# Kernel optimization log

Hardware: AMD Instinct MI355X
Metric: run time of the kernel (lower is better)

The kernel has to match this reference:

```python
import jax, jax.numpy as jnp
import numpy as np

B, SQ, SKV = 4, 4096, 1024
QDIM, CDIM = 1024, 768
HEADS, DHEAD = 16, 64
INNER = HEADS * DHEAD


def setup_inputs() -> dict:
    key = jax.random.key(0)
    ks = jax.random.split(key, 7)
    s = 0.02
    return {
        "x": jax.random.normal(ks[0], (B, SQ, QDIM), dtype=jnp.float32),
        "context": jax.random.normal(ks[1], (B, SKV, CDIM), dtype=jnp.float32),
        "Wq": jax.random.normal(ks[2], (QDIM, INNER), dtype=jnp.float32) * s,
        "Wk": jax.random.normal(ks[3], (CDIM, INNER), dtype=jnp.float32) * s,
        "Wv": jax.random.normal(ks[4], (CDIM, INNER), dtype=jnp.float32) * s,
        "Wo": jax.random.normal(ks[5], (INNER, QDIM), dtype=jnp.float32) * s,
        "bo": jnp.zeros((QDIM,), dtype=jnp.float32),
    }


def reference(x, context, Wq, Wk, Wv, Wo, bo):
    # QKV projections (no bias, matching bias=False Linear layers)
    q = x @ Wq          # [B, SQ, INNER]
    k = context @ Wk    # [B, SKV, INNER]
    v = context @ Wv    # [B, SKV, INNER]

    # split heads: b s (h d) -> b h s d
    def split_heads(t, s):
        return t.reshape(B, s, HEADS, DHEAD).transpose(0, 2, 1, 3)

    qh = split_heads(q, SQ)
    kh = split_heads(k, SKV)
    vh = split_heads(v, SKV)

    scale = DHEAD ** -0.5  # attention_basic default scale
    sim = jnp.einsum('bhqd,bhkd->bhqk', qh, kh) * scale  # [B,H,SQ,SKV]
    attn = jax.nn.softmax(sim, axis=-1)
    out = jnp.einsum('bhqk,bhkd->bhqd', attn, vh)        # [B,H,SQ,DHEAD]
    out = out.transpose(0, 2, 1, 3).reshape(B, SQ, INNER)

    # output projection (Linear with bias); dropout p=0 -> identity
    return out @ Wo + bo
```

## Files before the change

### kernel.cpp

```cpp
#include <hip/hip_runtime.h>


typedef unsigned short u16;
typedef __bf16 bf16x8 __attribute__((ext_vector_type(8)));
typedef float float4v __attribute__((ext_vector_type(4)));
typedef _Float16 half4 __attribute__((ext_vector_type(4)));
typedef _Float16 half2v __attribute__((ext_vector_type(2)));
typedef __attribute__((address_space(1))) void as1_void;
typedef __attribute__((address_space(3))) void as3_void;

__device__ __forceinline__ u16 f2bf(float f) {
  unsigned u = __float_as_uint(f);
  u += 0x7FFF + ((u >> 16) & 1);
  return (u16)(u >> 16);
}

__device__ __forceinline__ void async16(const u16* g, u16* l) {
  __builtin_amdgcn_global_load_lds((as1_void*)(void*)g, (as3_void*)l, 16, 0, 0);
}

#define WAITCNT_VM8 0xF78
#define WAITCNT_VM4 0xF74
#define WAITCNT_VM0 0xF70

__global__ void cvt_kernel(const float* __restrict__ x, u16* __restrict__ xbf,
                           const float* __restrict__ ctx, u16* __restrict__ ctxbf) {
  int i = blockIdx.x * 256 + threadIdx.x;
  const float* in; u16* out; int j;
  if (i < 4194304) { in = x; out = xbf; j = i; }
  else if (i < 4980736) { in = ctx; out = ctxbf; j = i - 4194304; }
  else return;
  float4 v = ((const float4*)in)[j];
  ushort4 o;
  o.x = f2bf(v.x); o.y = f2bf(v.y); o.z = f2bf(v.z); o.w = f2bf(v.w);
  ((ushort4*)out)[j] = o;
}

__global__ void twt_kernel(const float* __restrict__ Wq, const float* __restrict__ Wk,
                           const float* __restrict__ Wv, const float* __restrict__ Wo,
                           u16* __restrict__ WqT, u16* __restrict__ WkT,
                           u16* __restrict__ WvT, u16* __restrict__ WoT) {
  __shared__ u16 t[32][33];
  int z = blockIdx.z;
  const float* W = z == 0 ? Wq : z == 1 ? Wk : z == 2 ? Wv : Wo;
  u16* Wt = z == 0 ? WqT : z == 1 ? WkT : z == 2 ? WvT : WoT;
  int Kd = (z == 1 || z == 2) ? 768 : 1024;
  int k0 = blockIdx.y * 32;
  if (k0 >= Kd) return;
  int tx = threadIdx.x, ty = threadIdx.y;
  int n0 = blockIdx.x * 32;
#pragma unroll
  for (int i = 0; i < 4; i++)
    t[ty + i * 8][tx] = f2bf(W[(size_t)(k0 + ty + i * 8) * 1024 + n0 + tx]);
  __syncthreads();
#pragma unroll
  for (int i = 0; i < 4; i++)
    Wt[(size_t)(n0 + ty + i * 8) * Kd + k0 + tx] = t[tx][ty + i * 8];
}


__device__ __forceinline__ void ld_a4(const u16 (*Lp)[256][8], int rbase, int quad,
                                      int l15, bf16x8 a[4][2]) {
#pragma unroll
  for (int mi = 0; mi < 4; mi++)
#pragma unroll
    for (int ks = 0; ks < 2; ks++)
      a[mi][ks] = *(const bf16x8*)&Lp[ks * 4 + quad][rbase + mi * 16 + l15][0];
}

__device__ __forceinline__ void ld_b2(const u16 (*Lp)[256][8], int rbase, int quad,
                                      int l15, bf16x8 b[2][2]) {
#pragma unroll
  for (int ni = 0; ni < 2; ni++)
#pragma unroll
    for (int ks = 0; ks < 2; ks++)
      b[ni][ks] = *(const bf16x8*)&Lp[ks * 4 + quad][rbase + ni * 16 + l15][0];
}

__device__ __forceinline__ void mm16(bf16x8 a[4][2], bf16x8 b[2][2],
                                     float4v acc[8][4], int mh, int nh) {
  __builtin_amdgcn_s_setprio(1);
#pragma unroll
  for (int mi = 0; mi < 4; mi++)
#pragma unroll
    for (int ni = 0; ni < 2; ni++)
#pragma unroll
      for (int ks = 0; ks < 2; ks++)
        acc[mh * 4 + mi][nh * 2 + ni] = __builtin_amdgcn_mfma_f32_16x16x32_bf16(
            a[mi][ks], b[ni][ks], acc[mh * 4 + mi][nh * 2 + ni], 0, 0, 0);
  __builtin_amdgcn_s_setprio(0);
}

__device__ __forceinline__ void gemm256_core(const u16* __restrict__ A,
                                             const u16* __restrict__ Bt, int K,
                                             int m0, int n0, float4v acc[8][4]) {
  __shared__ __align__(16) u16 L[2][2][8][256][8];
  int tid = threadIdx.x;
  int w = tid >> 6, lane = tid & 63;
  int l15 = lane & 15, quad = lane >> 4;
  int wm = (w >> 2) * 128, wn = (w & 3) * 64;

  int c0 = 2 * w, c1 = 2 * w + 1;
  int kc0 = c0 & 7, mb0 = (c0 >> 3) * 64;
  int kc1 = c1 & 7, mb1 = (c1 >> 3) * 64;
  const u16* pA0 = A + (size_t)(m0 + mb0 + lane) * K + kc0 * 8;
  const u16* pA1 = A + (size_t)(m0 + mb1 + lane) * K + kc1 * 8;
  const u16* pB0 = Bt + (size_t)(n0 + mb0 + lane) * K + kc0 * 8;
  const u16* pB1 = Bt + (size_t)(n0 + mb1 + lane) * K + kc1 * 8;
  size_t hs = (size_t)128 * K;

#define STG_A(buf, t)                                                          \
  do {                                                                         \
    const u16* s0 = pA0 + (size_t)(t) * 64;                                    \
    const u16* s1 = pA1 + (size_t)(t) * 64;                                    \
    async16(s0, &L[buf][0][kc0][mb0][0]);                                      \
    async16(s1, &L[buf][0][kc1][mb1][0]);                                      \
    async16(s0 + hs, &L[buf][0][kc0][128 + mb0][0]);                           \
    async16(s1 + hs, &L[buf][0][kc1][128 + mb1][0]);                           \
  } while (0)
#define STG_B(buf, t)                                                          \
  do {                                                                         \
    const u16* s0 = pB0 + (size_t)(t) * 64;                                    \
    const u16* s1 = pB1 + (size_t)(t) * 64;                                    \
    async16(s0, &L[buf][1][kc0][mb0][0]);                                      \
    async16(s1, &L[buf][1][kc1][mb1][0]);                                      \
    async16(s0 + hs, &L[buf][1][kc0][128 + mb0][0]);                           \
    async16(s1 + hs, &L[buf][1][kc1][128 + mb1][0]);                           \
  } while (0)

  STG_A(0, 0); STG_B(0, 0);
  STG_A(1, 1); STG_B(1, 1);
  __builtin_amdgcn_s_waitcnt(WAITCNT_VM8);
  __builtin_amdgcn_s_barrier();

  bf16x8 a[4][2], b0[2][2], b1[2][2];
  int I = K >> 7;
  for (int i = 0; i < I; ++i) {
    int st = (i + 1 < I);
    ld_a4(L[0][0], wm, quad, l15, a);
    ld_b2(L[0][1], wn, quad, l15, b0);
    if (i > 0) STG_B(1, 2 * i + 1);
    __builtin_amdgcn_s_barrier();
    mm16(a, b0, acc, 0, 0);
    __builtin_amdgcn_s_barrier();
    ld_b2(L[0][1], wn + 32, quad, l15, b1);
    __builtin_amdgcn_s_barrier();
    mm16(a, b1, acc, 0, 1);
    __builtin_amdgcn_s_barrier();
    ld_a4(L[0][0], wm + 64, quad, l15, a);
    __builtin_amdgcn_s_barrier();
    mm16(a, b1, acc, 1, 1);
    __builtin_amdgcn_s_barrier();
    if (st) STG_A(0, 2 * i + 2);
    __builtin_amdgcn_s_barrier();
    mm16(a, b0, acc, 1, 0);
    if (st) __builtin_amdgcn_s_waitcnt(WAITCNT_VM4);
    else    __builtin_amdgcn_s_waitcnt(WAITCNT_VM0);
    __builtin_amdgcn_s_barrier();
    ld_a4(L[1][0], wm, quad, l15, a);
    ld_b2(L[1][1], wn, quad, l15, b0);
    if (st) STG_B(0, 2 * i + 2);
    __builtin_amdgcn_s_barrier();
    mm16(a, b0, acc, 0, 0);
    __builtin_amdgcn_s_barrier();
    ld_b2(L[1][1], wn + 32, quad, l15, b1);
    __builtin_amdgcn_s_barrier();
    mm16(a, b1, acc, 0, 1);
    __builtin_amdgcn_s_barrier();
    ld_a4(L[1][0], wm + 64, quad, l15, a);
    __builtin_amdgcn_s_barrier();
    mm16(a, b1, acc, 1, 1);
    __builtin_amdgcn_s_barrier();
    if (st) STG_A(1, 2 * i + 3);
    __builtin_amdgcn_s_barrier();
    mm16(a, b0, acc, 1, 0);
    if (st) __builtin_amdgcn_s_waitcnt(WAITCNT_VM4);
    __builtin_amdgcn_s_barrier();
  }
#undef STG_A
#undef STG_B
}

__global__ __launch_bounds__(512, 2) void qkv_gemm8(
    const u16* __restrict__ xbf, const u16* __restrict__ ctxbf,
    const u16* __restrict__ WqT, const u16* __restrict__ WkT, const u16* __restrict__ WvT,
    u16* __restrict__ Qb, u16* __restrict__ Kbuf, u16* __restrict__ Vtb, float qscale) {
  int bx = blockIdx.x;
  const u16* A; const u16* Bt; u16* C; int K, mode, m0, n0; float scale;
  if (bx < 256)      { int t = bx;       A = xbf;   Bt = WqT; C = Qb;   K = 1024; mode = 0; scale = qscale; m0 = (t >> 2) * 256; n0 = (t & 3) * 256; }
  else if (bx < 320) { int t = bx - 256; A = ctxbf; Bt = WkT; C = Kbuf; K = 768;  mode = 0; scale = 1.0f;   m0 = (t >> 2) * 256; n0 = (t & 3) * 256; }
  else               { int t = bx - 320; A = ctxbf; Bt = WvT; C = Vtb;  K = 768;  mode = 2; scale = 1.0f;   m0 = (t >> 2) * 256; n0 = (t & 3) * 256; }

  float4v acc[8][4] = {};
  gemm256_core(A, Bt, K, m0, n0, acc);

  int tid = threadIdx.x;
  int w = tid >> 6, lane = tid & 63;
  int l15 = lane & 15, quad = lane >> 4;
  int wm = (w >> 2) * 128, wn = (w & 3) * 64;

  if (mode == 0) {
#pragma unroll
    for (int mi = 0; mi < 8; mi++) {
      int rowb = m0 + wm + mi * 16 + quad * 4;
#pragma unroll
      for (int ni = 0; ni < 4; ni++) {
        int col = n0 + wn + ni * 16 + l15;
#pragma unroll
        for (int r = 0; r < 4; r++)
          C[(size_t)(rowb + r) * 1024 + col] = f2bf(acc[mi][ni][r] * scale);
      }
    }
  } else {
#pragma unroll
    for (int mi = 0; mi < 8; mi++) {
      int rowb = m0 + wm + mi * 16 + quad * 4;
#pragma unroll
      for (int ni = 0; ni < 4; ni++) {
        int col = n0 + wn + ni * 16 + l15;
        int hh = col >> 6, dd = col & 63;
#pragma unroll
        for (int r = 0; r < 4; r++) {
          int rr = rowb + r;
          int b = rr >> 10, skv = rr & 1023;
          _Float16 hv = (_Float16)acc[mi][ni][r];
          C[((((size_t)b * 16 + hh) * 64 + dd) << 10) + skv] = __builtin_bit_cast(u16, hv);
        }
      }
    }
  }
}

__global__ __launch_bounds__(512, 2) void gemm_bt8(
    const u16* __restrict__ A, const u16* __restrict__ Bt,
    float* __restrict__ C, const float* __restrict__ bias) {
  int bx = blockIdx.x;
  int m0 = (bx >> 2) * 256, n0 = (bx & 3) * 256;

  float4v acc[8][4] = {};
  gemm256_core(A, Bt, 1024, m0, n0, acc);

  int tid = threadIdx.x;
  int w = tid >> 6, lane = tid & 63;
  int l15 = lane & 15, quad = lane >> 4;
  int wm = (w >> 2) * 128, wn = (w & 3) * 64;

#pragma unroll
  for (int mi = 0; mi < 8; mi++) {
    int rowb = m0 + wm + mi * 16 + quad * 4;
#pragma unroll
    for (int ni = 0; ni < 4; ni++) {
      int col = n0 + wn + ni * 16 + l15;
      float bv = bias[col];
#pragma unroll
      for (int r = 0; r < 4; r++)
        C[(size_t)(rowb + r) * 1024 + col] = acc[mi][ni][r] + bv;
    }
  }
}

__global__ __launch_bounds__(512, 4) void attn_kernel(
    const u16* __restrict__ Q, const u16* __restrict__ Kb,
    const u16* __restrict__ Vt, u16* __restrict__ Oout) {
  __shared__ __align__(16) u16 lK[2][4096];
  __shared__ __align__(16) u16 lV[2][4096];
  int tid = threadIdx.x, w = tid >> 6, lane = tid & 63;
  int l15 = lane & 15, quad = lane >> 4;
  int bh = blockIdx.y, b = bh >> 4, h = bh & 15;
  int q0 = blockIdx.x * 256 + w * 32;

  const u16* Qbase = Q + ((size_t)(b * 4096 + q0)) * 1024 + h * 64;
  const u16* Kbase = Kb + ((size_t)b << 20) + h * 64;
  const u16* Vbase = Vt + ((size_t)bh << 16);

  bf16x8 qf[2][2];
#pragma unroll
  for (int qt = 0; qt < 2; qt++)
#pragma unroll
    for (int c = 0; c < 2; c++)
      qf[qt][c] = *(const bf16x8*)(Qbase + (size_t)(qt * 16 + l15) * 1024 + c * 32 + quad * 8);

  int x0 = ((tid & 7) ^ ((tid >> 3) & 7)) * 8, r0 = (tid >> 3) * 1024;
  const u16* ks0 = Kbase + r0 + x0;
  const u16* vs0 = Vbase + r0 + x0;
  int kdo0 = w * 512;

  async16(ks0, &lK[0][kdo0]);
  async16(vs0, &lV[0][kdo0]);
  ks0 += 65536;
  vs0 += 64;

  float4v o[2][4] = {};
  float4v osum[2] = {};
  const half4 ones = {(_Float16)1.0f, (_Float16)1.0f, (_Float16)1.0f, (_Float16)1.0f};

  int lb = l15 & 7;
  int xk0 = ((0 + quad) ^ lb) * 16 + l15 * 128;
  int xk1 = ((4 + quad) ^ lb) * 16 + l15 * 128;
  int qh = quad >> 1, qo = (quad & 1) * 8;
  int vrow = l15 * 128 + qo;

  for (int it = 0; it < 16; ++it) {
    const char* bK = (const char*)lK + (it & 1) * 8192;
    const char* bV = (const char*)lV + (it & 1) * 8192;
    __syncthreads();
    if (it < 15) {
      int nb = (it + 1) & 1;
      async16(ks0, &lK[nb][kdo0]);
      async16(vs0, &lV[nb][kdo0]);
      ks0 += 65536;
      vs0 += 64;
    }
#pragma unroll
    for (int ss = 0; ss < 4; ss++) {
      int sub = (ss + w) & 3;
      int sb = sub * 2048;
      float4v sv[2] = {{0.f, 0.f, 0.f, 0.f}, {0.f, 0.f, 0.f, 0.f}};
      __builtin_amdgcn_s_setprio(1);
#pragma unroll
      for (int c = 0; c < 2; c++) {
        bf16x8 kf = *(const bf16x8*)(bK + sb + (c ? xk1 : xk0));
#pragma unroll
        for (int qt = 0; qt < 2; qt++)
          sv[qt] = __builtin_amdgcn_mfma_f32_16x16x32_bf16(kf, qf[qt][c], sv[qt], 0, 0, 0);
      }
      __builtin_amdgcn_s_setprio(0);
      half4 pf[2];
#pragma unroll
      for (int qt = 0; qt < 2; qt++) {
        float e0 = exp2f(sv[qt][0]), e1 = exp2f(sv[qt][1]);
        float e2 = exp2f(sv[qt][2]), e3 = exp2f(sv[qt][3]);
        half2v p01 = __builtin_bit_cast(half2v, __builtin_amdgcn_cvt_pkrtz(e0, e1));
        half2v p23 = __builtin_bit_cast(half2v, __builtin_amdgcn_cvt_pkrtz(e2, e3));
        pf[qt] = __builtin_shufflevector(p01, p23, 0, 1, 2, 3);
        osum[qt] = __builtin_amdgcn_mfma_f32_16x16x16f16(ones, pf[qt], osum[qt], 0, 0, 0);
      }
      int vbs = vrow + (((sub * 2 + qh) ^ lb) * 16);
      __builtin_amdgcn_s_setprio(1);
#pragma unroll
      for (int dt = 0; dt < 4; dt++) {
        half4 vf = *(const half4*)(bV + dt * 2048 + vbs);
#pragma unroll
        for (int qt = 0; qt < 2; qt++)
          o[qt][dt] = __builtin_amdgcn_mfma_f32_16x16x16f16(vf, pf[qt], o[qt][dt], 0, 0, 0);
      }
      __builtin_amdgcn_s_setprio(0);
    }
  }

#pragma unroll
  for (int qt = 0; qt < 2; qt++) {
    float inv = 1.0f / osum[qt][0];
    u16* Ob = Oout + ((size_t)(b * 4096 + q0 + qt * 16 + l15)) * 1024 + h * 64 + quad * 4;
#pragma unroll
    for (int dt = 0; dt < 4; dt++) {
      ushort4 pk;
      pk.x = f2bf(o[qt][dt][0] * inv);
      pk.y = f2bf(o[qt][dt][1] * inv);
      pk.z = f2bf(o[qt][dt][2] * inv);
      pk.w = f2bf(o[qt][dt][3] * inv);
      *(ushort4*)(Ob + dt * 16) = pk;
    }
  }
}

extern "C" void kernel_launch(void* const* d_in, const int* in_sizes, int n_in,
                              void* d_out, int out_size, void* d_ws, size_t ws_size,
                              hipStream_t stream) {
  const float* x   = (const float*)d_in[0];
  const float* ctx = (const float*)d_in[1];
  const float* Wq  = (const float*)d_in[2];
  const float* Wk  = (const float*)d_in[3];
  const float* Wv  = (const float*)d_in[4];
  const float* Wo  = (const float*)d_in[5];
  const float* bo  = (const float*)d_in[6];
  float* out = (float*)d_out;

  u16* ws    = (u16*)d_ws;
  u16* xbf   = ws;
  u16* ctxbf = xbf + 16777216;
  u16* WqT   = ctxbf + 3145728;
  u16* WkT   = WqT + 1048576;
  u16* WvT   = WkT + 786432;
  u16* WoT   = WvT + 786432;
  u16* Qb    = WoT + 1048576;
  u16* Kbuf  = Qb + 16777216;
  u16* Vtb   = Kbuf + 4194304;
  if (ws_size < (size_t)48758784 * 2) return;

  cvt_kernel<<<19456, 256, 0, stream>>>(x, xbf, ctx, ctxbf);
  twt_kernel<<<dim3(32, 32, 4), dim3(32, 8), 0, stream>>>(Wq, Wk, Wv, Wo, WqT, WkT, WvT, WoT);
  qkv_gemm8<<<dim3(384), dim3(512), 0, stream>>>(xbf, ctxbf, WqT, WkT, WvT,
                                                 Qb, Kbuf, Vtb, 0.18033688011112042f);
  attn_kernel<<<dim3(16, 64), dim3(512), 0, stream>>>(Qb, Kbuf, Vtb, xbf);
  gemm_bt8<<<dim3(256), dim3(512), 0, stream>>>(xbf, WoT, out, bo);
}
```

Baseline: 395.2 us.

## Use 16x16x32 f16 MFMA for PV by permuting P fragments across lanes

Pairs of 16-key subtiles are merged so the P@V and row-sum products use the K=32 f16 MFMA instead of two K=16 MFMAs. Since the QK output layout does not match the K=32 operand layout, P values are rearranged across lanes with ds_bpermute and a per-lane select, and V is loaded as 8-wide fragments. This halves the number of PV MFMA issues but adds 16 bpermutes per step. It also drops the per-wave staggered subtile order.

```diff
diff --git a/kernel.cpp b/kernel.cpp
--- a/kernel.cpp
+++ b/kernel.cpp
@@ -2,10 +2,14 @@
 
 
 typedef unsigned short u16;
+typedef unsigned int u32;
 typedef __bf16 bf16x8 __attribute__((ext_vector_type(8)));
 typedef float float4v __attribute__((ext_vector_type(4)));
 typedef _Float16 half4 __attribute__((ext_vector_type(4)));
+typedef _Float16 half8 __attribute__((ext_vector_type(8)));
 typedef _Float16 half2v __attribute__((ext_vector_type(2)));
+typedef u32 u32x2 __attribute__((ext_vector_type(2)));
+typedef u32 u32x4 __attribute__((ext_vector_type(4)));
 typedef __attribute__((address_space(1))) void as1_void;
 typedef __attribute__((address_space(3))) void as3_void;
 
@@ -292,13 +296,16 @@
 
   float4v o[2][4] = {};
   float4v osum[2] = {};
-  const half4 ones = {(_Float16)1.0f, (_Float16)1.0f, (_Float16)1.0f, (_Float16)1.0f};
+  const half8 ones8 = {(_Float16)1.0f, (_Float16)1.0f, (_Float16)1.0f, (_Float16)1.0f,
+                       (_Float16)1.0f, (_Float16)1.0f, (_Float16)1.0f, (_Float16)1.0f};
 
   int lb = l15 & 7;
   int xk0 = ((0 + quad) ^ lb) * 16 + l15 * 128;
   int xk1 = ((4 + quad) ^ lb) * 16 + l15 * 128;
-  int qh = quad >> 1, qo = (quad & 1) * 8;
-  int vrow = l15 * 128 + qo;
+  int vrow = l15 * 128;
+  int idx_lo = (((quad & 1) << 5) + l15) << 2;
+  int idx_hi = idx_lo + 64;
+  bool useb = (quad & 2) != 0;
 
   for (int it = 0; it < 16; ++it) {
     const char* bK = (const char*)lK + (it & 1) * 8192;
@@ -312,37 +319,60 @@
       vs0 += 64;
     }
 #pragma unroll
-    for (int ss = 0; ss < 4; ss++) {
-      int sub = (ss + w) & 3;
-      int sb = sub * 2048;
-      float4v sv[2] = {{0.f, 0.f, 0.f, 0.f}, {0.f, 0.f, 0.f, 0.f}};
+    for (int s = 0; s < 2; ++s) {
+      half4 pp[2][2];
+#pragma unroll
+      for (int hp = 0; hp < 2; ++hp) {
+        int sub = s * 2 + hp;
+        const char* kb = bK + sub * 2048;
+        float4v sv[2] = {{0.f, 0.f, 0.f, 0.f}, {0.f, 0.f, 0.f, 0.f}};
+        __builtin_amdgcn_s_setprio(1);
+#pragma unroll
+        for (int c = 0; c < 2; c++) {
+          bf16x8 kf = *(const bf16x8*)(kb + (c ? xk1 : xk0));
+#pragma unroll
+          for (int qt = 0; qt < 2; qt++)
+            sv[qt] = __builtin_amdgcn_mfma_f32_16x16x32_bf16(kf, qf[qt][c], sv[qt], 0, 0, 0);
+        }
+        __builtin_amdgcn_s_setprio(0);
+#pragma unroll
+        for (int qt = 0; qt < 2; qt++) {
+          float e0 = exp2f(sv[qt][0]), e1 = exp2f(sv[qt][1]);
+          float e2 = exp2f(sv[qt][2]), e3 = exp2f(sv[qt][3]);
+          half2v p01 = __builtin_bit_cast(half2v, __builtin_amdgcn_cvt_pkrtz(e0, e1));
+          half2v p23 = __builtin_bit_cast(half2v, __builtin_amdgcn_cvt_pkrtz(e2, e3));
+          pp[hp][qt] = __builtin_shufflevector(p01, p23, 0, 1, 2, 3);
+        }
+      }
+      half8 p8s[2];
+#pragma unroll
+      for (int qt = 0; qt < 2; qt++) {
+        u32x2 a2 = __builtin_bit_cast(u32x2, pp[0][qt]);
+        u32x2 b2 = __builtin_bit_cast(u32x2, pp[1][qt]);
+        int al0 = __builtin_amdgcn_ds_bpermute(idx_lo, (int)a2[0]);
+        int ah0 = __builtin_amdgcn_ds_bpermute(idx_lo, (int)a2[1]);
+        int al1 = __builtin_amdgcn_ds_bpermute(idx_hi, (int)a2[0]);
+        int ah1 = __builtin_amdgcn_ds_bpermute(idx_hi, (int)a2[1]);
+        int bl0 = __builtin_amdgcn_ds_bpermute(idx_lo, (int)b2[0]);
+        int bh0 = __builtin_amdgcn_ds_bpermute(idx_lo, (int)b2[1]);
+        int bl1 = __builtin_amdgcn_ds_bpermute(idx_hi, (int)b2[0]);
+        int bh1 = __builtin_amdgcn_ds_bpermute(idx_hi, (int)b2[1]);
+        u32x4 od;
+        od[0] = (u32)(useb ? bl0 : al0);
+        od[1] = (u32)(useb ? bh0 : ah0);
+        od[2] = (u32)(useb ? bl1 : al1);
+        od[3] = (u32)(useb ? bh1 : ah1);
+        half8 p8 = __builtin_bit_cast(half8, od);
+        p8s[qt] = p8;
+        osum[qt] = __builtin_amdgcn_mfma_f32_16x16x32_f16(ones8, p8, osum[qt], 0, 0, 0);
+      }
       __builtin_amdgcn_s_setprio(1);
 #pragma unroll
-      for (int c = 0; c < 2; c++) {
-        bf16x8 kf = *(const bf16x8*)(bK + sb + (c ? xk1 : xk0));
+      for (int dt = 0; dt < 4; dt++) {
+        half8 vf = *(const half8*)(bV + dt * 2048 + vrow + (((s * 4 + quad) ^ lb) * 16));
 #pragma unroll
         for (int qt = 0; qt < 2; qt++)
-          sv[qt] = __builtin_amdgcn_mfma_f32_16x16x32_bf16(kf, qf[qt][c], sv[qt], 0, 0, 0);
-      }
-      __builtin_amdgcn_s_setprio(0);
-      half4 pf[2];
-#pragma unroll
-      for (int qt = 0; qt < 2; qt++) {
-        float e0 = exp2f(sv[qt][0]), e1 = exp2f(sv[qt][1]);
-        float e2 = exp2f(sv[qt][2]), e3 = exp2f(sv[qt][3]);
-        half2v p01 = __builtin_bit_cast(half2v, __builtin_amdgcn_cvt_pkrtz(e0, e1));
-        half2v p23 = __builtin_bit_cast(half2v, __builtin_amdgcn_cvt_pkrtz(e2, e3));
-        pf[qt] = __builtin_shufflevector(p01, p23, 0, 1, 2, 3);
-        osum[qt] = __builtin_amdgcn_mfma_f32_16x16x16f16(ones, pf[qt], osum[qt], 0, 0, 0);
-      }
-      int vbs = vrow + (((sub * 2 + qh) ^ lb) * 16);
-      __builtin_amdgcn_s_setprio(1);
-#pragma unroll
-      for (int dt = 0; dt < 4; dt++) {
-        half4 vf = *(const half4*)(bV + dt * 2048 + vbs);
-#pragma unroll
-        for (int qt = 0; qt < 2; qt++)
-          o[qt][dt] = __builtin_amdgcn_mfma_f32_16x16x16f16(vf, pf[qt], o[qt][dt], 0, 0, 0);
+          o[qt][dt] = __builtin_amdgcn_mfma_f32_16x16x32_f16(vf, p8s[qt], o[qt][dt], 0, 0, 0);
       }
       __builtin_amdgcn_s_setprio(0);
     }
```

Result: no change. 390.8 us (-1.1%).

## Double KV tile per iteration in attention kernel to halve barrier count

Applied to the files above, without the earlier changes.

The attention kernel now stages 128 keys/values per iteration instead of 64, doubling the LDS buffers and halving the outer loop count and the matching __syncthreads barriers. The V tile layout and its XOR swizzle change to 16-way, to suit the wider rows. This amortises synchronisation and async-load issue overhead over more MFMA work. In exchange, LDS use grows to 64KB per block, which may lower occupancy below the requested 4 blocks per CU.

```diff
diff --git a/kernel.cpp b/kernel.cpp
--- a/kernel.cpp
+++ b/kernel.cpp
@@ -2,6 +2,7 @@
 
 
 typedef unsigned short u16;
+typedef unsigned int u32;
 typedef __bf16 bf16x8 __attribute__((ext_vector_type(8)));
 typedef float float4v __attribute__((ext_vector_type(4)));
 typedef _Float16 half4 __attribute__((ext_vector_type(4)));
@@ -262,8 +263,8 @@
 __global__ __launch_bounds__(512, 4) void attn_kernel(
     const u16* __restrict__ Q, const u16* __restrict__ Kb,
     const u16* __restrict__ Vt, u16* __restrict__ Oout) {
-  __shared__ __align__(16) u16 lK[2][4096];
-  __shared__ __align__(16) u16 lV[2][4096];
+  __shared__ __align__(16) u16 lK[2][8192];
+  __shared__ __align__(16) u16 lV[2][8192];
   int tid = threadIdx.x, w = tid >> 6, lane = tid & 63;
   int l15 = lane & 15, quad = lane >> 4;
   int bh = blockIdx.y, b = bh >> 4, h = bh & 15;
@@ -280,15 +281,18 @@
     for (int c = 0; c < 2; c++)
       qf[qt][c] = *(const bf16x8*)(Qbase + (size_t)(qt * 16 + l15) * 1024 + c * 32 + quad * 8);
 
-  int x0 = ((tid & 7) ^ ((tid >> 3) & 7)) * 8, r0 = (tid >> 3) * 1024;
-  const u16* ks0 = Kbase + r0 + x0;
-  const u16* vs0 = Vbase + r0 + x0;
-  int kdo0 = w * 512;
-
-  async16(ks0, &lK[0][kdo0]);
-  async16(vs0, &lV[0][kdo0]);
-  ks0 += 65536;
-  vs0 += 64;
+  int kr0 = tid >> 3, kx0 = ((tid & 7) ^ (kr0 & 7)) * 8;
+  const u16* ks0 = Kbase + (size_t)kr0 * 1024 + kx0;
+  const u16* ks1 = ks0 + (size_t)64 * 1024;
+  int vd0 = tid >> 4, vc0 = ((tid & 15) ^ (vd0 & 15)) * 8;
+  const u16* vs0 = Vbase + (size_t)vd0 * 1024 + vc0;
+  const u16* vs1 = vs0 + (size_t)32 * 1024;
+  int kdo0 = w * 512, kdo1 = 4096 + w * 512;
+
+  async16(ks0, &lK[0][kdo0]); async16(ks1, &lK[0][kdo1]);
+  async16(vs0, &lV[0][kdo0]); async16(vs1, &lV[0][kdo1]);
+  ks0 += 131072; ks1 += 131072;
+  vs0 += 128; vs1 += 128;
 
   float4v o[2][4] = {};
   float4v osum[2] = {};
@@ -298,22 +302,22 @@
   int xk0 = ((0 + quad) ^ lb) * 16 + l15 * 128;
   int xk1 = ((4 + quad) ^ lb) * 16 + l15 * 128;
   int qh = quad >> 1, qo = (quad & 1) * 8;
-  int vrow = l15 * 128 + qo;
-
-  for (int it = 0; it < 16; ++it) {
-    const char* bK = (const char*)lK + (it & 1) * 8192;
-    const char* bV = (const char*)lV + (it & 1) * 8192;
+  int vrow = l15 * 256 + qo;
+
+  for (int it = 0; it < 8; ++it) {
+    const char* bK = (const char*)lK + (it & 1) * 16384;
+    const char* bV = (const char*)lV + (it & 1) * 16384;
     __syncthreads();
-    if (it < 15) {
+    if (it < 7) {
       int nb = (it + 1) & 1;
-      async16(ks0, &lK[nb][kdo0]);
-      async16(vs0, &lV[nb][kdo0]);
-      ks0 += 65536;
-      vs0 += 64;
-    }
-#pragma unroll
-    for (int ss = 0; ss < 4; ss++) {
-      int sub = (ss + w) & 3;
+      async16(ks0, &lK[nb][kdo0]); async16(ks1, &lK[nb][kdo1]);
+      async16(vs0, &lV[nb][kdo0]); async16(vs1, &lV[nb][kdo1]);
+      ks0 += 131072; ks1 += 131072;
+      vs0 += 128; vs1 += 128;
+    }
+#pragma unroll
+    for (int ss = 0; ss < 8; ss++) {
+      int sub = (ss + w) & 7;
       int sb = sub * 2048;
       float4v sv[2] = {{0.f, 0.f, 0.f, 0.f}, {0.f, 0.f, 0.f, 0.f}};
       __builtin_amdgcn_s_setprio(1);
@@ -335,11 +339,11 @@
         pf[qt] = __builtin_shufflevector(p01, p23, 0, 1, 2, 3);
         osum[qt] = __builtin_amdgcn_mfma_f32_16x16x16f16(ones, pf[qt], osum[qt], 0, 0, 0);
       }
-      int vbs = vrow + (((sub * 2 + qh) ^ lb) * 16);
+      int vbs = vrow + (((sub * 2 + qh) ^ l15) * 16);
       __builtin_amdgcn_s_setprio(1);
 #pragma unroll
       for (int dt = 0; dt < 4; dt++) {
-        half4 vf = *(const half4*)(bV + dt * 2048 + vbs);
+        half4 vf = *(const half4*)(bV + dt * 4096 + vbs);
 #pragma unroll
         for (int qt = 0; qt < 2; qt++)
           o[qt][dt] = __builtin_amdgcn_mfma_f32_16x16x16f16(vf, pf[qt], o[qt][dt], 0, 0, 0);
```

After: 378.3 us. 4.3% less time.
